# Optimization experiments

Measured on AMD Instinct MI355X. Metric: run time of the kernel, lower is better.

The kernel has to match this reference:

```python
import jax, jax.numpy as jnp
import numpy as np

DIM = 128
LAYERS = 3
N_NODES = 50000
N_EDGES = 640000
LN_EPS = 1e-5


def setup_inputs() -> dict:
    key = jax.random.key(0)
    ks = jax.random.split(key, 10)
    s = 1.0 / np.sqrt(DIM)
    x = jax.random.normal(ks[0], (N_NODES, DIM), dtype=jnp.float32)
    edge_index = jax.random.randint(ks[1], (2, N_EDGES), 0, N_NODES, dtype=jnp.int64)
    in_w = jax.random.uniform(ks[2], (DIM, DIM), jnp.float32, -s, s)
    in_b = jax.random.uniform(ks[3], (DIM,), jnp.float32, -s, s)
    w1 = jax.random.uniform(ks[4], (LAYERS, DIM, DIM), jnp.float32, -s, s)
    b1 = jax.random.uniform(ks[5], (LAYERS, DIM), jnp.float32, -s, s)
    w2 = jax.random.uniform(ks[6], (LAYERS, DIM, DIM), jnp.float32, -s, s)
    b2 = jax.random.uniform(ks[7], (LAYERS, DIM), jnp.float32, -s, s)
    ln_g = jnp.ones((LAYERS, DIM), jnp.float32)
    ln_b = jnp.zeros((LAYERS, DIM), jnp.float32)
    return {"x": x, "edge_index": edge_index, "in_w": in_w, "in_b": in_b,
            "w1": w1, "b1": b1, "w2": w2, "b2": b2, "ln_g": ln_g, "ln_b": ln_b}


def _layer_norm(z, g, b):
    mu = jnp.mean(z, axis=-1, keepdims=True)
    var = jnp.mean(jnp.square(z - mu), axis=-1, keepdims=True)
    return (z - mu) * jax.lax.rsqrt(var + LN_EPS) * g + b


def reference(x, edge_index, in_w, in_b, w1, b1, w2, b2, ln_g, ln_b):
    src, dst = edge_index[0], edge_index[1]
    n = x.shape[0]
    # degree is identical every layer in the original; compute once (same math)
    deg = jax.ops.segment_sum(jnp.ones(dst.shape, x.dtype), dst, num_segments=n)
    deg = jnp.maximum(deg, 1.0)[:, None]  # [N,1]
    h = x @ in_w + in_b  # [N,D]
    for i in range(w1.shape[0]):
        m = jax.ops.segment_sum(h[src], dst, num_segments=n) / deg  # gather+scatter
        mlp = jax.nn.relu(m @ w1[i] + b1[i]) @ w2[i] + b2[i]
        h = _layer_norm(h + mlp, ln_g[i], ln_b[i])
    return h
```

## Files before the change

### kernel.cpp

```cpp
#include <hip/hip_runtime.h>

#define DIM 128
#define LN_EPS 1e-5f

typedef __attribute__((ext_vector_type(8))) short s16x8;
typedef __attribute__((ext_vector_type(4))) float f32x4;
typedef __attribute__((ext_vector_type(4))) unsigned int u32x4;

__device__ __forceinline__ unsigned short f2bf(float f) {
    unsigned u = __float_as_uint(f);
    unsigned r = u + 0x7fffu + ((u >> 16) & 1u);
    return (unsigned short)(r >> 16);
}
__device__ __forceinline__ float bf2f(unsigned short b) {
    return __uint_as_float(((unsigned)b) << 16);
}


__global__ void count_deg(const int* __restrict__ dst, int E, int* __restrict__ counts) {
    int i = blockIdx.x * 256 + threadIdx.x;
    if (i < E) atomicAdd(&counts[dst[i]], 1);
}

__global__ __launch_bounds__(256) void scan_partials(const int* __restrict__ counts, int n,
                                                     int* __restrict__ bsum) {
    int base = blockIdx.x * 1024 + threadIdx.x * 4;
    int s = 0;
#pragma unroll
    for (int j = 0; j < 4; ++j) {
        int i = base + j;
        if (i < n) s += counts[i];
    }
#pragma unroll
    for (int off = 32; off > 0; off >>= 1) s += __shfl_xor(s, off, 64);
    __shared__ int wsum[4];
    int lane = threadIdx.x & 63, wid = threadIdx.x >> 6;
    if (lane == 0) wsum[wid] = s;
    __syncthreads();
    if (threadIdx.x == 0) bsum[blockIdx.x] = wsum[0] + wsum[1] + wsum[2] + wsum[3];
}

__global__ __launch_bounds__(64) void scan_bsums(const int* __restrict__ bsum,
                                                 int* __restrict__ bofs, int nb,
                                                 int* __restrict__ rowptr, int N, int E) {
    int lane = threadIdx.x;
    int carry = 0;
    for (int base = 0; base < nb; base += 64) {
        int v = (base + lane < nb) ? bsum[base + lane] : 0;
        int incl = v;
#pragma unroll
        for (int off = 1; off < 64; off <<= 1) {
            int t = __shfl_up(incl, off, 64);
            if (lane >= off) incl += t;
        }
        if (base + lane < nb) bofs[base + lane] = carry + incl - v;
        carry += __shfl(incl, 63, 64);
    }
    if (lane == 0) rowptr[N] = E;
}

__global__ __launch_bounds__(256) void scan_final(const int* __restrict__ counts, int n,
                                                  const int* __restrict__ bofs,
                                                  int* __restrict__ rowptr,
                                                  int* __restrict__ cursor,
                                                  float* __restrict__ dinv) {
    int base = blockIdx.x * 1024 + threadIdx.x * 4;
    int v[4];
#pragma unroll
    for (int j = 0; j < 4; ++j) {
        int i = base + j;
        v[j] = (i < n) ? counts[i] : 0;
    }
    int tsum = v[0] + v[1] + v[2] + v[3];
    int lane = threadIdx.x & 63, wid = threadIdx.x >> 6;
    int incl = tsum;
#pragma unroll
    for (int off = 1; off < 64; off <<= 1) {
        int t = __shfl_up(incl, off, 64);
        if (lane >= off) incl += t;
    }
    __shared__ int wsum[4];
    if (lane == 63) wsum[wid] = incl;
    __syncthreads();
    int wofs = 0;
    for (int w = 0; w < 4; ++w)
        if (w < wid) wofs += wsum[w];
    int excl = bofs[blockIdx.x] + wofs + (incl - tsum);
#pragma unroll
    for (int j = 0; j < 4; ++j) {
        int i = base + j;
        if (i < n) {
            rowptr[i] = excl;
            cursor[i] = excl;
            dinv[i] = 1.0f / (float)((v[j] > 1) ? v[j] : 1);
            excl += v[j];
        }
    }
}

__global__ void fill_csr(const int* __restrict__ src, const int* __restrict__ dst, int E,
                         int* __restrict__ cursor, int* __restrict__ srcidx) {
    int i = blockIdx.x * 256 + threadIdx.x;
    if (i < E) {
        int p = atomicAdd(&cursor[dst[i]], 1);
        srcidx[p] = src[i];
    }
}


__global__ __launch_bounds__(256) void cvt_weights(const float* __restrict__ in_w,
                                                   const float* __restrict__ w1,
                                                   const float* __restrict__ w2,
                                                   unsigned short* __restrict__ wt, int L) {
    int mat = blockIdx.x >> 3, part = blockIdx.x & 7;
    const float* src;
    if (mat == 0) src = in_w;
    else if (mat <= L) src = w1 + (size_t)(mat - 1) * DIM * DIM;
    else src = w2 + (size_t)(mat - 1 - L) * DIM * DIM;
    unsigned short* dst = wt + (size_t)mat * DIM * DIM;
    int base = part * 2048 + threadIdx.x;
#pragma unroll
    for (int j = 0; j < 8; ++j) {
        int i = base + j * 256;
        int k = i >> 7, n = i & 127;
        dst[n * DIM + k] = f2bf(src[i]);
    }
}


__global__ __launch_bounds__(256) void gemm_bias_mfma(const float* __restrict__ x,
                                                      const unsigned short* __restrict__ Wt,
                                                      const float* __restrict__ bias,
                                                      unsigned short* __restrict__ hb, int N) {
    int tid = threadIdx.x;
    int s = tid >> 6, lane = tid & 63;
    int quad = lane >> 4, l16 = lane & 15;
    int r0 = blockIdx.x * 16;
    int cs = s * 32;
    int arow = r0 + l16;
    bool av = arow < N;

    f32x4 acc[2];
    acc[0] = (f32x4){0.f, 0.f, 0.f, 0.f};
    acc[1] = (f32x4){0.f, 0.f, 0.f, 0.f};

    const float4* xp = (const float4*)(x + ((size_t)(av ? arow : 0) << 7)) + quad * 2;
#pragma unroll
    for (int k0 = 0; k0 < 128; k0 += 32) {
        s16x8 a = {0, 0, 0, 0, 0, 0, 0, 0};
        if (av) {
            float4 f0 = xp[k0 / 4];
            float4 f1 = xp[k0 / 4 + 1];
            a[0] = (short)f2bf(f0.x); a[1] = (short)f2bf(f0.y);
            a[2] = (short)f2bf(f0.z); a[3] = (short)f2bf(f0.w);
            a[4] = (short)f2bf(f1.x); a[5] = (short)f2bf(f1.y);
            a[6] = (short)f2bf(f1.z); a[7] = (short)f2bf(f1.w);
        }
        s16x8 b0 = *(const s16x8*)(Wt + ((size_t)(cs + l16) << 7) + quad * 8 + k0);
        s16x8 b1 = *(const s16x8*)(Wt + ((size_t)(cs + 16 + l16) << 7) + quad * 8 + k0);
        acc[0] = __builtin_amdgcn_mfma_f32_16x16x32_bf16(a, b0, acc[0], 0, 0, 0);
        acc[1] = __builtin_amdgcn_mfma_f32_16x16x32_bf16(a, b1, acc[1], 0, 0, 0);
    }

#pragma unroll
    for (int c = 0; c < 2; ++c) {
        int col = cs + c * 16 + l16;
        float bv = bias[col];
#pragma unroll
        for (int reg = 0; reg < 4; ++reg) {
            int grow = r0 + quad * 4 + reg;
            if (grow < N) hb[((size_t)grow << 7) + col] = f2bf(acc[c][reg] + bv);
        }
    }
}


__global__ __launch_bounds__(256) void agg_mlp_ln(const unsigned short* __restrict__ hin,
                                                  const int* __restrict__ rowptr,
                                                  const int* __restrict__ srcidx,
                                                  const float* __restrict__ dinv,
                                                  const unsigned short* __restrict__ W1t,
                                                  const float* __restrict__ B1,
                                                  const unsigned short* __restrict__ W2t,
                                                  const float* __restrict__ B2,
                                                  const float* __restrict__ G,
                                                  const float* __restrict__ Bb,
                                                  unsigned short* __restrict__ hout,
                                                  float* __restrict__ out_f32, int N) {
    __shared__ unsigned short M[16][132];
    __shared__ unsigned short P[16][132];
    __shared__ float s1p[4][16], s2p[4][16];

    int tid = threadIdx.x;
    int s = tid >> 6, lane = tid & 63;
    int quad = lane >> 4, l16 = lane & 15;
    int g = lane >> 2, li = lane & 3;
    int r0 = blockIdx.x * 16;
    int cs = s * 32;

    int nd = r0 + g;
    bool nv = nd < N;
    int e  = nv ? rowptr[nd] : 0;
    int ee = nv ? rowptr[nd + 1] : 0;

    float a0[8] = {0, 0, 0, 0, 0, 0, 0, 0};
    float a1[8] = {0, 0, 0, 0, 0, 0, 0, 0};
    const unsigned short* hsl = hin + cs + li * 8;

    while (__any(e < ee)) {
        int myidx = (e + li < ee) ? srcidx[e + li] : 0;
        int i0 = __shfl(myidx, (g << 2) | 0, 64);
        int i1 = __shfl(myidx, (g << 2) | 1, 64);
        int i2 = __shfl(myidx, (g << 2) | 2, 64);
        int i3 = __shfl(myidx, (g << 2) | 3, 64);
        bool p0 = e < ee, p1 = e + 1 < ee, p2 = e + 2 < ee, p3 = e + 3 < ee;
        u32x4 v0, v1, v2, v3;
        if (p0) v0 = *(const u32x4*)(hsl + ((size_t)i0 << 7));
        if (p1) v1 = *(const u32x4*)(hsl + ((size_t)i1 << 7));
        if (p2) v2 = *(const u32x4*)(hsl + ((size_t)i2 << 7));
        if (p3) v3 = *(const u32x4*)(hsl + ((size_t)i3 << 7));
        if (p0) {
#pragma unroll
            for (int j = 0; j < 4; ++j) {
                a0[2 * j]     += __uint_as_float(v0[j] << 16);
                a0[2 * j + 1] += __uint_as_float(v0[j] & 0xffff0000u);
            }
        }
        if (p1) {
#pragma unroll
            for (int j = 0; j < 4; ++j) {
                a1[2 * j]     += __uint_as_float(v1[j] << 16);
                a1[2 * j + 1] += __uint_as_float(v1[j] & 0xffff0000u);
            }
        }
        if (p2) {
#pragma unroll
            for (int j = 0; j < 4; ++j) {
                a0[2 * j]     += __uint_as_float(v2[j] << 16);
                a0[2 * j + 1] += __uint_as_float(v2[j] & 0xffff0000u);
            }
        }
        if (p3) {
#pragma unroll
            for (int j = 0; j < 4; ++j) {
                a1[2 * j]     += __uint_as_float(v3[j] << 16);
                a1[2 * j + 1] += __uint_as_float(v3[j] & 0xffff0000u);
            }
        }
        e += 4;
    }

    {
        float di = nv ? dinv[nd] : 0.f;
        u32x4 o;
#pragma unroll
        for (int j = 0; j < 4; ++j) {
            unsigned lo = f2bf((a0[2 * j] + a1[2 * j]) * di);
            unsigned hi = f2bf((a0[2 * j + 1] + a1[2 * j + 1]) * di);
            o[j] = lo | (hi << 16);
        }
        *(u32x4*)(&M[g][cs + li * 8]) = o;
    }
    __syncthreads();

    f32x4 acc[2];
    acc[0] = (f32x4){0.f, 0.f, 0.f, 0.f};
    acc[1] = (f32x4){0.f, 0.f, 0.f, 0.f};
#pragma unroll
    for (int k0 = 0; k0 < 128; k0 += 32) {
        s16x8 a = *(const s16x8*)(&M[l16][quad * 8 + k0]);
        s16x8 b0 = *(const s16x8*)(W1t + ((size_t)(cs + l16) << 7) + quad * 8 + k0);
        s16x8 b1 = *(const s16x8*)(W1t + ((size_t)(cs + 16 + l16) << 7) + quad * 8 + k0);
        acc[0] = __builtin_amdgcn_mfma_f32_16x16x32_bf16(a, b0, acc[0], 0, 0, 0);
        acc[1] = __builtin_amdgcn_mfma_f32_16x16x32_bf16(a, b1, acc[1], 0, 0, 0);
    }
#pragma unroll
    for (int c = 0; c < 2; ++c) {
        int col = cs + c * 16 + l16;
        float bv = B1[col];
#pragma unroll
        for (int reg = 0; reg < 4; ++reg) {
            float v = fmaxf(acc[c][reg] + bv, 0.f);
            P[quad * 4 + reg][col] = f2bf(v);
        }
    }
    __syncthreads();

    acc[0] = (f32x4){0.f, 0.f, 0.f, 0.f};
    acc[1] = (f32x4){0.f, 0.f, 0.f, 0.f};
#pragma unroll
    for (int k0 = 0; k0 < 128; k0 += 32) {
        s16x8 a = *(const s16x8*)(&P[l16][quad * 8 + k0]);
        s16x8 b0 = *(const s16x8*)(W2t + ((size_t)(cs + l16) << 7) + quad * 8 + k0);
        s16x8 b1 = *(const s16x8*)(W2t + ((size_t)(cs + 16 + l16) << 7) + quad * 8 + k0);
        acc[0] = __builtin_amdgcn_mfma_f32_16x16x32_bf16(a, b0, acc[0], 0, 0, 0);
        acc[1] = __builtin_amdgcn_mfma_f32_16x16x32_bf16(a, b1, acc[1], 0, 0, 0);
    }

    float z[2][4];
    float ps1[4] = {0, 0, 0, 0}, ps2[4] = {0, 0, 0, 0};
#pragma unroll
    for (int c = 0; c < 2; ++c) {
        int col = cs + c * 16 + l16;
        float b2v = B2[col];
#pragma unroll
        for (int reg = 0; reg < 4; ++reg) {
            int grow = r0 + quad * 4 + reg;
            float hv = (grow < N) ? bf2f(hin[((size_t)grow << 7) + col]) : 0.f;
            float zz = acc[c][reg] + b2v + hv;
            z[c][reg] = zz;
            ps1[reg] += zz;
            ps2[reg] += zz * zz;
        }
    }
#pragma unroll
    for (int off = 1; off < 16; off <<= 1) {
#pragma unroll
        for (int reg = 0; reg < 4; ++reg) {
            ps1[reg] += __shfl_xor(ps1[reg], off, 64);
            ps2[reg] += __shfl_xor(ps2[reg], off, 64);
        }
    }
    if (l16 == 0) {
#pragma unroll
        for (int reg = 0; reg < 4; ++reg) {
            s1p[s][quad * 4 + reg] = ps1[reg];
            s2p[s][quad * 4 + reg] = ps2[reg];
        }
    }
    __syncthreads();

#pragma unroll
    for (int reg = 0; reg < 4; ++reg) {
        int row = quad * 4 + reg;
        float S1 = s1p[0][row] + s1p[1][row] + s1p[2][row] + s1p[3][row];
        float S2 = s2p[0][row] + s2p[1][row] + s2p[2][row] + s2p[3][row];
        float mean = S1 * (1.0f / 128.0f);
        float var = S2 * (1.0f / 128.0f) - mean * mean;
        float rs = rsqrtf(var + LN_EPS);
        int grow = r0 + row;
        if (grow < N) {
#pragma unroll
            for (int c = 0; c < 2; ++c) {
                int col = cs + c * 16 + l16;
                float o = (z[c][reg] - mean) * rs * G[col] + Bb[col];
                hout[((size_t)grow << 7) + col] = f2bf(o);
                if (out_f32) out_f32[((size_t)grow << 7) + col] = o;
            }
        }
    }
}


extern "C" void kernel_launch(void* const* d_in, const int* in_sizes, int n_in,
                              void* d_out, int out_size, void* d_ws, size_t ws_size,
                              hipStream_t stream) {
    const float* x    = (const float*)d_in[0];
    const int*   ei   = (const int*)d_in[1];
    const float* in_w = (const float*)d_in[2];
    const float* in_b = (const float*)d_in[3];
    const float* w1   = (const float*)d_in[4];
    const float* b1   = (const float*)d_in[5];
    const float* w2   = (const float*)d_in[6];
    const float* b2   = (const float*)d_in[7];
    const float* ln_g = (const float*)d_in[8];
    const float* ln_b = (const float*)d_in[9];

    const int N = in_sizes[0] / DIM;
    const int E = in_sizes[1] / 2;
    const int LAYERS = in_sizes[4] / (DIM * DIM);

    const int* e_src = ei;
    const int* e_dst = ei + E;

    char* ws = (char*)d_ws;
    unsigned short* hb0    = (unsigned short*)ws;  ws += (size_t)N * DIM * 2;
    unsigned short* hb1    = (unsigned short*)ws;  ws += (size_t)N * DIM * 2;
    int*            counts = (int*)ws;             ws += (size_t)N * 4;
    int*            rowptr = (int*)ws;             ws += (size_t)(N + 1) * 4;
    int*            cursor = (int*)ws;             ws += (size_t)N * 4;
    float*          dinv   = (float*)ws;           ws += (size_t)N * 4;
    int*            srcidx = (int*)ws;             ws += (size_t)E * 4;
    int*            bsum   = (int*)ws;             ws += 4096;
    int*            bofs   = (int*)ws;             ws += 4096;
    unsigned short* wt     = (unsigned short*)ws;  ws += (size_t)(2 * LAYERS + 1) * DIM * DIM * 2;

    const int nScanBlocks = (N + 1023) / 1024;
    const int nMat = 2 * LAYERS + 1;

    hipMemsetAsync(counts, 0, (size_t)N * 4, stream);
    count_deg<<<(E + 255) / 256, 256, 0, stream>>>(e_dst, E, counts);
    scan_partials<<<nScanBlocks, 256, 0, stream>>>(counts, N, bsum);
    scan_bsums<<<1, 64, 0, stream>>>(bsum, bofs, nScanBlocks, rowptr, N, E);
    scan_final<<<nScanBlocks, 256, 0, stream>>>(counts, N, bofs, rowptr, cursor, dinv);
    fill_csr<<<(E + 255) / 256, 256, 0, stream>>>(e_src, e_dst, E, cursor, srcidx);
    cvt_weights<<<nMat * 8, 256, 0, stream>>>(in_w, w1, w2, wt, LAYERS);

    const unsigned short* in_wt = wt;
    const unsigned short* w1t   = wt + (size_t)DIM * DIM;
    const unsigned short* w2t   = wt + (size_t)(1 + LAYERS) * DIM * DIM;

    int tile_grid = (N + 15) / 16;
    gemm_bias_mfma<<<tile_grid, 256, 0, stream>>>(x, in_wt, in_b, hb0, N);

    unsigned short* hin = hb0;
    unsigned short* hout = hb1;
    for (int i = 0; i < LAYERS; ++i) {
        float* out = (i == LAYERS - 1) ? (float*)d_out : nullptr;
        agg_mlp_ln<<<tile_grid, 256, 0, stream>>>(hin, rowptr, srcidx, dinv,
                                                  w1t + (size_t)i * DIM * DIM, b1 + (size_t)i * DIM,
                                                  w2t + (size_t)i * DIM * DIM, b2 + (size_t)i * DIM,
                                                  ln_g + (size_t)i * DIM, ln_b + (size_t)i * DIM,
                                                  hout, out, N);
        unsigned short* t = hin; hin = hout; hout = t;
    }
}
```

Baseline: 369.4 us.

## Gather neighbor features in FP8 and fuse the three-kernel scan into one

Each layer now writes an FP8 E4M3 copy of the hidden state alongside the bf16 copy. The neighbor gather-sum reads that FP8 copy, halving the bytes fetched per edge in the memory-bound aggregation, with an extra byte-wide store per element as the cost. FP8 also loses precision in the aggregated messages, which risks accuracy. Separately, the three-kernel prefix scan for CSR construction is replaced by one 1024-thread block, removing two launches but serializing the scan on a single workgroup.

New measurement: 484.7 us. 31.2% more time.

```diff
diff --git a/kernel.cpp b/kernel.cpp
--- a/kernel.cpp
+++ b/kernel.cpp
@@ -1,11 +1,14 @@
 #include <hip/hip_runtime.h>
+#include <hip/hip_fp8.h>
 
 #define DIM 128
 #define LN_EPS 1e-5f
 
 typedef __attribute__((ext_vector_type(8))) short s16x8;
 typedef __attribute__((ext_vector_type(4))) float f32x4;
+typedef __attribute__((ext_vector_type(2))) float f32x2;
 typedef __attribute__((ext_vector_type(4))) unsigned int u32x4;
+typedef __attribute__((ext_vector_type(2))) unsigned int u32x2;
 
 __device__ __forceinline__ unsigned short f2bf(float f) {
     unsigned u = __float_as_uint(f);
@@ -15,6 +18,14 @@
 __device__ __forceinline__ float bf2f(unsigned short b) {
     return __uint_as_float(((unsigned)b) << 16);
 }
+__device__ __forceinline__ unsigned char f2fp8(float f) {
+    return (unsigned char)__hip_cvt_float_to_fp8(f, __HIP_SATFINITE, __HIP_E4M3);
+}
+__device__ __forceinline__ void acc_fp8x4(float* a, unsigned v) {
+    f32x2 lo = __builtin_amdgcn_cvt_pk_f32_fp8(v, false);
+    f32x2 hi = __builtin_amdgcn_cvt_pk_f32_fp8(v, true);
+    a[0] += lo[0]; a[1] += lo[1]; a[2] += hi[0]; a[3] += hi[1];
+}
 
 
 __global__ void count_deg(const int* __restrict__ dst, int E, int* __restrict__ counts) {
@@ -22,80 +33,43 @@
     if (i < E) atomicAdd(&counts[dst[i]], 1);
 }
 
-__global__ __launch_bounds__(256) void scan_partials(const int* __restrict__ counts, int n,
-                                                     int* __restrict__ bsum) {
-    int base = blockIdx.x * 1024 + threadIdx.x * 4;
+__global__ __launch_bounds__(1024) void scan_fused(const int* __restrict__ counts, int n, int E,
+                                                   int* __restrict__ rowptr,
+                                                   int* __restrict__ cursor,
+                                                   float* __restrict__ dinv) {
+    int t = threadIdx.x;
+    const int C = (n + 1023) / 1024;
+    int base = t * C;
     int s = 0;
-#pragma unroll
-    for (int j = 0; j < 4; ++j) {
+    for (int j = 0; j < C; ++j) {
         int i = base + j;
         if (i < n) s += counts[i];
     }
-#pragma unroll
-    for (int off = 32; off > 0; off >>= 1) s += __shfl_xor(s, off, 64);
-    __shared__ int wsum[4];
-    int lane = threadIdx.x & 63, wid = threadIdx.x >> 6;
-    if (lane == 0) wsum[wid] = s;
-    __syncthreads();
-    if (threadIdx.x == 0) bsum[blockIdx.x] = wsum[0] + wsum[1] + wsum[2] + wsum[3];
-}
-
-__global__ __launch_bounds__(64) void scan_bsums(const int* __restrict__ bsum,
-                                                 int* __restrict__ bofs, int nb,
-                                                 int* __restrict__ rowptr, int N, int E) {
-    int lane = threadIdx.x;
-    int carry = 0;
-    for (int base = 0; base < nb; base += 64) {
-        int v = (base + lane < nb) ? bsum[base + lane] : 0;
-        int incl = v;
-#pragma unroll
-        for (int off = 1; off < 64; off <<= 1) {
-            int t = __shfl_up(incl, off, 64);
-            if (lane >= off) incl += t;
-        }
-        if (base + lane < nb) bofs[base + lane] = carry + incl - v;
-        carry += __shfl(incl, 63, 64);
-    }
-    if (lane == 0) rowptr[N] = E;
-}
-
-__global__ __launch_bounds__(256) void scan_final(const int* __restrict__ counts, int n,
-                                                  const int* __restrict__ bofs,
-                                                  int* __restrict__ rowptr,
-                                                  int* __restrict__ cursor,
-                                                  float* __restrict__ dinv) {
-    int base = blockIdx.x * 1024 + threadIdx.x * 4;
-    int v[4];
-#pragma unroll
-    for (int j = 0; j < 4; ++j) {
-        int i = base + j;
-        v[j] = (i < n) ? counts[i] : 0;
-    }
-    int tsum = v[0] + v[1] + v[2] + v[3];
-    int lane = threadIdx.x & 63, wid = threadIdx.x >> 6;
-    int incl = tsum;
+    int lane = t & 63, wv = t >> 6;
+    int incl = s;
 #pragma unroll
     for (int off = 1; off < 64; off <<= 1) {
-        int t = __shfl_up(incl, off, 64);
-        if (lane >= off) incl += t;
-    }
-    __shared__ int wsum[4];
-    if (lane == 63) wsum[wid] = incl;
+        int tmp = __shfl_up(incl, off, 64);
+        if (lane >= off) incl += tmp;
+    }
+    __shared__ int wsum[16];
+    if (lane == 63) wsum[wv] = incl;
     __syncthreads();
     int wofs = 0;
-    for (int w = 0; w < 4; ++w)
-        if (w < wid) wofs += wsum[w];
-    int excl = bofs[blockIdx.x] + wofs + (incl - tsum);
-#pragma unroll
-    for (int j = 0; j < 4; ++j) {
+#pragma unroll
+    for (int w = 0; w < 16; ++w) wofs += (w < wv) ? wsum[w] : 0;
+    int excl = wofs + incl - s;
+    for (int j = 0; j < C; ++j) {
         int i = base + j;
         if (i < n) {
+            int v = counts[i];
             rowptr[i] = excl;
             cursor[i] = excl;
-            dinv[i] = 1.0f / (float)((v[j] > 1) ? v[j] : 1);
-            excl += v[j];
-        }
-    }
+            dinv[i] = 1.0f / (float)((v > 1) ? v : 1);
+            excl += v;
+        }
+    }
+    if (t == 0) rowptr[n] = E;
 }
 
 __global__ void fill_csr(const int* __restrict__ src, const int* __restrict__ dst, int E,
@@ -131,7 +105,8 @@
 __global__ __launch_bounds__(256) void gemm_bias_mfma(const float* __restrict__ x,
                                                       const unsigned short* __restrict__ Wt,
                                                       const float* __restrict__ bias,
-                                                      unsigned short* __restrict__ hb, int N) {
+                                                      unsigned short* __restrict__ hb,
+                                                      unsigned char* __restrict__ h8, int N) {
     int tid = threadIdx.x;
     int s = tid >> 6, lane = tid & 63;
     int quad = lane >> 4, l16 = lane & 15;
@@ -169,13 +144,18 @@
 #pragma unroll
         for (int reg = 0; reg < 4; ++reg) {
             int grow = r0 + quad * 4 + reg;
-            if (grow < N) hb[((size_t)grow << 7) + col] = f2bf(acc[c][reg] + bv);
+            if (grow < N) {
+                float o = acc[c][reg] + bv;
+                hb[((size_t)grow << 7) + col] = f2bf(o);
+                h8[((size_t)grow << 7) + col] = f2fp8(o);
+            }
         }
     }
 }
 
 
 __global__ __launch_bounds__(256) void agg_mlp_ln(const unsigned short* __restrict__ hin,
+                                                  const unsigned char* __restrict__ h8in,
                                                   const int* __restrict__ rowptr,
                                                   const int* __restrict__ srcidx,
                                                   const float* __restrict__ dinv,
@@ -186,6 +166,7 @@
                                                   const float* __restrict__ G,
                                                   const float* __restrict__ Bb,
                                                   unsigned short* __restrict__ hout,
+                                                  unsigned char* __restrict__ h8out,
                                                   float* __restrict__ out_f32, int N) {
     __shared__ unsigned short M[16][132];
     __shared__ unsigned short P[16][132];
@@ -205,7 +186,7 @@
 
     float a0[8] = {0, 0, 0, 0, 0, 0, 0, 0};
     float a1[8] = {0, 0, 0, 0, 0, 0, 0, 0};
-    const unsigned short* hsl = hin + cs + li * 8;
+    const unsigned char* hsl = h8in + cs + li * 8;
 
     while (__any(e < ee)) {
         int myidx = (e + li < ee) ? srcidx[e + li] : 0;
@@ -214,39 +195,15 @@
         int i2 = __shfl(myidx, (g << 2) | 2, 64);
         int i3 = __shfl(myidx, (g << 2) | 3, 64);
         bool p0 = e < ee, p1 = e + 1 < ee, p2 = e + 2 < ee, p3 = e + 3 < ee;
-        u32x4 v0, v1, v2, v3;
-        if (p0) v0 = *(const u32x4*)(hsl + ((size_t)i0 << 7));
-        if (p1) v1 = *(const u32x4*)(hsl + ((size_t)i1 << 7));
-        if (p2) v2 = *(const u32x4*)(hsl + ((size_t)i2 << 7));
-        if (p3) v3 = *(const u32x4*)(hsl + ((size_t)i3 << 7));
-        if (p0) {
-#pragma unroll
-            for (int j = 0; j < 4; ++j) {
-                a0[2 * j]     += __uint_as_float(v0[j] << 16);
-                a0[2 * j + 1] += __uint_as_float(v0[j] & 0xffff0000u);
-            }
-        }
-        if (p1) {
-#pragma unroll
-            for (int j = 0; j < 4; ++j) {
-                a1[2 * j]     += __uint_as_float(v1[j] << 16);
-                a1[2 * j + 1] += __uint_as_float(v1[j] & 0xffff0000u);
-            }
-        }
-        if (p2) {
-#pragma unroll
-            for (int j = 0; j < 4; ++j) {
-                a0[2 * j]     += __uint_as_float(v2[j] << 16);
-                a0[2 * j + 1] += __uint_as_float(v2[j] & 0xffff0000u);
-            }
-        }
-        if (p3) {
-#pragma unroll
-            for (int j = 0; j < 4; ++j) {
-                a1[2 * j]     += __uint_as_float(v3[j] << 16);
-                a1[2 * j + 1] += __uint_as_float(v3[j] & 0xffff0000u);
-            }
-        }
+        u32x2 v0, v1, v2, v3;
+        if (p0) v0 = *(const u32x2*)(hsl + ((size_t)i0 << 7));
+        if (p1) v1 = *(const u32x2*)(hsl + ((size_t)i1 << 7));
+        if (p2) v2 = *(const u32x2*)(hsl + ((size_t)i2 << 7));
+        if (p3) v3 = *(const u32x2*)(hsl + ((size_t)i3 << 7));
+        if (p0) { acc_fp8x4(a0,     v0[0]); acc_fp8x4(a0 + 4, v0[1]); }
+        if (p1) { acc_fp8x4(a1,     v1[0]); acc_fp8x4(a1 + 4, v1[1]); }
+        if (p2) { acc_fp8x4(a0,     v2[0]); acc_fp8x4(a0 + 4, v2[1]); }
+        if (p3) { acc_fp8x4(a1,     v3[0]); acc_fp8x4(a1 + 4, v3[1]); }
         e += 4;
     }
 
@@ -255,7 +212,7 @@
         u32x4 o;
 #pragma unroll
         for (int j = 0; j < 4; ++j) {
-            unsigned lo = f2bf((a0[2 * j] + a1[2 * j]) * di);
+            unsigned lo = f2bf((a0[2 * j]     + a1[2 * j])     * di);
             unsigned hi = f2bf((a0[2 * j + 1] + a1[2 * j + 1]) * di);
             o[j] = lo | (hi << 16);
         }
@@ -344,8 +301,12 @@
             for (int c = 0; c < 2; ++c) {
                 int col = cs + c * 16 + l16;
                 float o = (z[c][reg] - mean) * rs * G[col] + Bb[col];
-                hout[((size_t)grow << 7) + col] = f2bf(o);
-                if (out_f32) out_f32[((size_t)grow << 7) + col] = o;
+                if (out_f32) {
+                    out_f32[((size_t)grow << 7) + col] = o;
+                } else {
+                    hout[((size_t)grow << 7) + col] = f2bf(o);
+                    h8out[((size_t)grow << 7) + col] = f2fp8(o);
+                }
             }
         }
     }
@@ -376,23 +337,20 @@
     char* ws = (char*)d_ws;
     unsigned short* hb0    = (unsigned short*)ws;  ws += (size_t)N * DIM * 2;
     unsigned short* hb1    = (unsigned short*)ws;  ws += (size_t)N * DIM * 2;
+    unsigned char*  h8a    = (unsigned char*)ws;   ws += (size_t)N * DIM;
+    unsigned char*  h8b    = (unsigned char*)ws;   ws += (size_t)N * DIM;
     int*            counts = (int*)ws;             ws += (size_t)N * 4;
     int*            rowptr = (int*)ws;             ws += (size_t)(N + 1) * 4;
     int*            cursor = (int*)ws;             ws += (size_t)N * 4;
     float*          dinv   = (float*)ws;           ws += (size_t)N * 4;
     int*            srcidx = (int*)ws;             ws += (size_t)E * 4;
-    int*            bsum   = (int*)ws;             ws += 4096;
-    int*            bofs   = (int*)ws;             ws += 4096;
     unsigned short* wt     = (unsigned short*)ws;  ws += (size_t)(2 * LAYERS + 1) * DIM * DIM * 2;
 
-    const int nScanBlocks = (N + 1023) / 1024;
     const int nMat = 2 * LAYERS + 1;
 
-    hipMemsetAsync(counts, 0, (size_t)N * 4, stream);
+    (void)hipMemsetAsync(counts, 0, (size_t)N * 4, stream);
     count_deg<<<(E + 255) / 256, 256, 0, stream>>>(e_dst, E, counts);
-    scan_partials<<<nScanBlocks, 256, 0, stream>>>(counts, N, bsum);
-    scan_bsums<<<1, 64, 0, stream>>>(bsum, bofs, nScanBlocks, rowptr, N, E);
-    scan_final<<<nScanBlocks, 256, 0, stream>>>(counts, N, bofs, rowptr, cursor, dinv);
+    scan_fused<<<1, 1024, 0, stream>>>(counts, N, E, rowptr, cursor, dinv);
     fill_csr<<<(E + 255) / 256, 256, 0, stream>>>(e_src, e_dst, E, cursor, srcidx);
     cvt_weights<<<nMat * 8, 256, 0, stream>>>(in_w, w1, w2, wt, LAYERS);
 
@@ -401,17 +359,18 @@
     const unsigned short* w2t   = wt + (size_t)(1 + LAYERS) * DIM * DIM;
 
     int tile_grid = (N + 15) / 16;
-    gemm_bias_mfma<<<tile_grid, 256, 0, stream>>>(x, in_wt, in_b, hb0, N);
-
-    unsigned short* hin = hb0;
-    unsigned short* hout = hb1;
+    gemm_bias_mfma<<<tile_grid, 256, 0, stream>>>(x, in_wt, in_b, hb0, h8a, N);
+
+    unsigned short* hin  = hb0;  unsigned char* h8in  = h8a;
+    unsigned short* hout = hb1;  unsigned char* h8out = h8b;
     for (int i = 0; i < LAYERS; ++i) {
         float* out = (i == LAYERS - 1) ? (float*)d_out : nullptr;
-        agg_mlp_ln<<<tile_grid, 256, 0, stream>>>(hin, rowptr, srcidx, dinv,
+        agg_mlp_ln<<<tile_grid, 256, 0, stream>>>(hin, h8in, rowptr, srcidx, dinv,
                                                   w1t + (size_t)i * DIM * DIM, b1 + (size_t)i * DIM,
                                                   w2t + (size_t)i * DIM * DIM, b2 + (size_t)i * DIM,
                                                   ln_g + (size_t)i * DIM, ln_b + (size_t)i * DIM,
-                                                  hout, out, N);
+                                                  hout, h8out, out, N);
         unsigned short* t = hin; hin = hout; hout = t;
-    }
-}
+        unsigned char* t8 = h8in; h8in = h8out; h8out = t8;
+    }
+}
```
